# Kernel optimization log

Measured on AMD Instinct MI355X. Metric: run time of the kernel, lower is better.

## Reference

```python
import jax, jax.numpy as jnp
import numpy as np

N_LEVELS = 16
N_FEATS = 2
LOG2_T = 19
TABLE_SIZE = 2 ** LOG2_T
BASE_RES = 16
PER_LEVEL_SCALE = 1.3819
N_PTS = 524288
# per-level grid resolutions (static)
RESOLUTIONS = np.floor(BASE_RES * PER_LEVEL_SCALE ** np.arange(N_LEVELS)).astype(np.float32)
# NGP spatial hash primes for 2D
PRIME0 = np.uint32(1)
PRIME1 = np.uint32(2654435761)
# corner offsets for bilinear interp: (0,0),(0,1),(1,0),(1,1)
CORNER_OFFS = np.array([[0, 0], [0, 1], [1, 0], [1, 1]], dtype=np.uint32)


def setup_inputs() -> dict:
    key = jax.random.key(0)
    k1, k2 = jax.random.split(key)
    pts = jax.random.uniform(k1, (N_PTS, 3), dtype=jnp.float32)  # coords in [0,1]
    # 3 planes x L levels x T entries x F features, small init like NGP (1e-4)
    tables = jax.random.normal(k2, (3, N_LEVELS, TABLE_SIZE, N_FEATS), dtype=jnp.float32) * 1e-4
    return {"pts": pts, "tables": tables}


def _encode_plane(coords, table):
    # coords: [N,2] in [0,1]; table: [L,T,F]
    L, T, F = table.shape
    res = jnp.asarray(RESOLUTIONS)  # [L]
    scaled = coords[None, :, :] * res[:, None, None]  # [L,N,2]
    x0 = jnp.floor(scaled)
    frac = scaled - x0  # [L,N,2]
    x0u = x0.astype(jnp.uint32)
    offs = jnp.asarray(CORNER_OFFS)  # [4,2]
    corners = x0u[:, :, None, :] + offs[None, None, :, :]  # [L,N,4,2]
    # NGP spatial hash with uint32 wraparound, then mod table size
    h = (corners[..., 0] * PRIME0) ^ (corners[..., 1] * PRIME1)  # [L,N,4] uint32
    idx = (h % jnp.uint32(T)).astype(jnp.int32)  # [L,N,4]
    feats = table[jnp.arange(L)[:, None, None], idx]  # [L,N,4,F]
    # bilinear weights: product over dims of frac (offset=1) or 1-frac (offset=0)
    fo = offs.astype(coords.dtype)  # [4,2]
    w = jnp.prod(jnp.where(fo[None, None] > 0, frac[:, :, None, :], 1.0 - frac[:, :, None, :]), axis=-1)  # [L,N,4]
    out = jnp.einsum('lnc,lncf->lnf', w, feats)  # [L,N,F]
    return out.transpose(1, 0, 2).reshape(coords.shape[0], L * F)  # [N, L*F]


def reference(pts, tables):
    # coordinate-pair planes: combinations of (0,1,2) taken 2 at a time
    coo_combs = [(0, 1), (0, 2), (1, 2)]
    interp_space = 1.0
    for ci, comb in enumerate(coo_combs):
        interp_space = interp_space * _encode_plane(pts[:, list(comb)], tables[ci])
    return interp_space  # [N, 32]
```

## Files before the change

### kernel.cpp

```cpp
#include <hip/hip_runtime.h>
#include <stdint.h>


#define NPTS   524288u
#define TSIZE  524288u
#define TMASK  0x7FFFFu
#define PRIME1 2654435761u

__constant__ float c_res[16] = {
    16.f, 22.f, 30.f, 42.f, 58.f, 80.f, 111.f, 153.f,
    212.f, 294.f, 406.f, 561.f, 775.f, 1072.f, 1481.f, 2047.f
};
__constant__ int c_resiLow[12] = {16, 22, 30, 42, 58, 80, 111, 153, 212, 294, 406, 561};

__global__ __launch_bounds__(256) void k_pack(
    const float* __restrict__ pts, float2* __restrict__ pts2,
    uint32_t* __restrict__ hist)
{
    const uint32_t b = blockIdx.x, t = threadIdx.x;
    if (b == 2048u) {
        if (t < 256u) { hist[t] = 0u; hist[256u + t] = 0u; hist[512u + t] = 0u; }
        return;
    }
    const uint32_t pt = b * 256u + t;
    const float x = pts[pt * 3u + 0u];
    const float y = pts[pt * 3u + 1u];
    const float z = pts[pt * 3u + 2u];
    pts2[            pt] = make_float2(x, y);
    pts2[NPTS      + pt] = make_float2(x, z);
    pts2[2u * NPTS + pt] = make_float2(y, z);
}

__global__ __launch_bounds__(256) void k_hist(
    const float2* __restrict__ pts2, uint32_t* __restrict__ hist)
{
    __shared__ uint32_t lh[256];
    const uint32_t b = blockIdx.x, t = threadIdx.x;
    const uint32_t plane = b >> 6, chunk = b & 63u;
    lh[t] = 0u;
    __syncthreads();
    const float2* __restrict__ pp = pts2 + (size_t)plane * NPTS;
    const uint32_t pt0 = chunk * 8192u + t;
    for (uint32_t k = 0; k < 32u; ++k) {
        const float2 c = pp[pt0 + k * 256u];
        const uint32_t bx = min(15u, (uint32_t)(c.x * 16.f));
        const uint32_t by = min(15u, (uint32_t)(c.y * 16.f));
        atomicAdd(&lh[bx * 16u + by], 1u);
    }
    __syncthreads();
    atomicAdd(&hist[plane * 256u + t], lh[t]);
}

__global__ __launch_bounds__(256) void k_scan(
    const uint32_t* __restrict__ hist,
    uint32_t* __restrict__ base, uint32_t* __restrict__ cursor)
{
    __shared__ uint32_t su[256];
    const uint32_t t = threadIdx.x;
    for (uint32_t p = 0; p < 3u; ++p) {
        const uint32_t h = hist[p * 256u + t];
        su[t] = h;
        __syncthreads();
        for (uint32_t off = 1u; off < 256u; off <<= 1) {
            uint32_t v = 0u;
            if (t >= off) v = su[t - off];
            __syncthreads();
            su[t] += v;
            __syncthreads();
        }
        const uint32_t ex = su[t] - h;
        base[p * 256u + t] = ex;
        cursor[p * 256u + t] = ex;
        __syncthreads();
    }
}

__global__ __launch_bounds__(256) void k_scatter(
    const float2* __restrict__ pts2, uint32_t* __restrict__ cursor,
    float4* __restrict__ sort16)
{
    __shared__ uint32_t lcnt[256], gb[256], lc2[256];
    const uint32_t b = blockIdx.x, t = threadIdx.x;
    const uint32_t plane = b >> 6, chunk = b & 63u;
    lcnt[t] = 0u; lc2[t] = 0u;
    __syncthreads();
    const float2* __restrict__ pp = pts2 + (size_t)plane * NPTS;
    const uint32_t pt0 = chunk * 8192u + t;
    for (uint32_t k = 0; k < 32u; ++k) {
        const float2 c = pp[pt0 + k * 256u];
        const uint32_t bb = min(15u, (uint32_t)(c.x * 16.f)) * 16u
                          + min(15u, (uint32_t)(c.y * 16.f));
        atomicAdd(&lcnt[bb], 1u);
    }
    __syncthreads();
    gb[t] = atomicAdd(&cursor[plane * 256u + t], lcnt[t]);
    __syncthreads();
    float4* __restrict__ sp = sort16 + (size_t)plane * NPTS;
    for (uint32_t k = 0; k < 32u; ++k) {
        const uint32_t pt = pt0 + k * 256u;
        const float2 c = pp[pt];
        const uint32_t bb = min(15u, (uint32_t)(c.x * 16.f)) * 16u
                          + min(15u, (uint32_t)(c.y * 16.f));
        const uint32_t r = atomicAdd(&lc2[bb], 1u);
        sp[gb[bb] + r] = make_float4(c.x, c.y, __uint_as_float(pt), 0.f);
    }
}

__global__ __launch_bounds__(256) void k_low(
    const float2* __restrict__ tab, const float4* __restrict__ sort16,
    const uint32_t* __restrict__ hist, const uint32_t* __restrict__ base,
    float2* __restrict__ ws2)
{
    __shared__ float2 sm[4000];
    __shared__ uint32_t Poff[12], Pu0[12], Pu1[12], Pcols[12], Prows[12];
    const uint32_t b = blockIdx.x, t = threadIdx.x;
    const uint32_t plane = b >> 8, bucket = b & 255u;
    const uint32_t bx = bucket >> 4, by = bucket & 15u;

    if (t == 0u) {
        uint32_t off = 0u;
        for (uint32_t l = 0; l < 12u; ++l) {
            const int R = c_resiLow[l];
            const int u0s = max(0, (int)(((int)bx * R) >> 4) - 1);
            const int u0e = min(R, (int)((((int)bx + 1) * R) >> 4) + 2);
            const int u1s = max(0, (int)(((int)by * R) >> 4) - 1);
            const int u1e = min(R, (int)((((int)by + 1) * R) >> 4) + 2);
            const uint32_t rows = (uint32_t)(u0e - u0s + 1);
            const uint32_t cols = (uint32_t)(u1e - u1s + 1);
            Poff[l] = off; Pu0[l] = (uint32_t)u0s; Pu1[l] = (uint32_t)u1s;
            Pcols[l] = cols; Prows[l] = rows;
            off += rows * cols;
        }
    }
    __syncthreads();

    for (uint32_t l = 0; l < 12u; ++l) {
        const uint32_t E = Prows[l] * Pcols[l];
        const uint32_t cols = Pcols[l], u0s = Pu0[l], u1s = Pu1[l];
        const uint32_t tb = (plane * 16u + l) * TSIZE;
        for (uint32_t i = t; i < E; i += 256u) {
            const uint32_t cx = u0s + i / cols;
            const uint32_t cy = u1s + i - (i / cols) * cols;
            sm[Poff[l] + i] = tab[tb + ((cx ^ (cy * PRIME1)) & TMASK)];
        }
    }
    __syncthreads();

    const uint32_t count = hist[plane * 256u + bucket];
    const uint32_t start = base[plane * 256u + bucket];
    const float4* __restrict__ sp = sort16 + (size_t)plane * NPTS;
    float4* __restrict__ w4 = (float4*)ws2;

    for (uint32_t i = t; i < count; i += 256u) {
        const float4 f = sp[start + i];
        const float c0 = f.x, c1 = f.y;
        const uint32_t orig = __float_as_uint(f.z);
        float2 acc[12];
#pragma unroll
        for (int l = 0; l < 12; ++l) {
            const float res = c_res[l];
            const float s0 = c0 * res;
            const float s1 = c1 * res;
            const float f0 = floorf(s0);
            const float f1 = floorf(s1);
            const float r0 = s0 - f0;
            const float r1 = s1 - f1;
            const uint32_t u0 = (uint32_t)f0, u1 = (uint32_t)f1;
            const uint32_t ci = Poff[l] + (u0 - Pu0[l]) * Pcols[l] + (u1 - Pu1[l]);
            const float2 q00 = sm[ci];
            const float2 q01 = sm[ci + 1u];
            const float2 q10 = sm[ci + Pcols[l]];
            const float2 q11 = sm[ci + Pcols[l] + 1u];
            const float w00 = (1.f - r0) * (1.f - r1);
            const float w01 = (1.f - r0) * r1;
            const float w10 = r0 * (1.f - r1);
            const float w11 = r0 * r1;
            acc[l] = make_float2(
                w00 * q00.x + w01 * q01.x + w10 * q10.x + w11 * q11.x,
                w00 * q00.y + w01 * q01.y + w10 * q10.y + w11 * q11.y);
        }
        const size_t d = (size_t)orig * 18u + (size_t)plane * 6u;
        w4[d + 0] = make_float4(acc[0].x, acc[0].y, acc[1].x, acc[1].y);
        w4[d + 1] = make_float4(acc[2].x, acc[2].y, acc[3].x, acc[3].y);
        w4[d + 2] = make_float4(acc[4].x, acc[4].y, acc[5].x, acc[5].y);
        w4[d + 3] = make_float4(acc[6].x, acc[6].y, acc[7].x, acc[7].y);
        w4[d + 4] = make_float4(acc[8].x, acc[8].y, acc[9].x, acc[9].y);
        w4[d + 5] = make_float4(acc[10].x, acc[10].y, acc[11].x, acc[11].y);
    }
}

__global__ __launch_bounds__(256) void k_hi(
    const float2* __restrict__ pts2, const float2* __restrict__ tab,
    float2* __restrict__ wsH)
{
    const uint32_t b = blockIdx.x, t = threadIdx.x;
    const uint32_t xcd = b & 7u;
    const uint32_t s   = b >> 3;
    uint32_t g, chunk;
    if (s < 512u) { g = xcd; chunk = s; }
    else { g = 8u + (xcd >> 1); chunk = ((xcd & 1u) << 8) + (s - 512u); }
    const uint32_t plane = g % 3u;
    const uint32_t lvl   = 12u + g / 3u;
    const uint32_t gabs  = plane * 16u + lvl;
    const float    res   = c_res[lvl];
    const uint32_t tb    = gabs * TSIZE;
    const float4* __restrict__ tab4 = (const float4*)tab;
    const uint32_t b4    = gabs * (TSIZE / 2u);
    const float2* __restrict__ pp = pts2 + (size_t)plane * NPTS;
    const uint32_t pt0   = chunk * 1024u + t;

    float4 P0[4], P1[4];
    float2 Q0[4], Q1[4];
    float  r0[4], r1[4];
    uint32_t sel0[4], sel1[4], oddm[4];

#pragma unroll
    for (int k = 0; k < 4; ++k) {
        const uint32_t pt = pt0 + (uint32_t)k * 256u;
        const float2 c2 = pp[pt];
        const float s0 = c2.x * res;
        const float s1 = c2.y * res;
        const float f0 = floorf(s0);
        const float f1 = floorf(s1);
        r0[k] = s0 - f0;
        r1[k] = s1 - f1;
        const uint32_t u0  = (uint32_t)f0;
        const uint32_t hy0 = (uint32_t)f1 * PRIME1;
        const uint32_t hy1 = hy0 + PRIME1;
        const uint32_t i00 = ( u0        ^ hy0) & TMASK;
        const uint32_t i01 = ( u0        ^ hy1) & TMASK;
        const uint32_t i10 = ((u0 + 1u)  ^ hy0) & TMASK;
        const uint32_t i11 = ((u0 + 1u)  ^ hy1) & TMASK;
        sel0[k] = i00 & 1u;
        sel1[k] = i01 & 1u;
        oddm[k] = u0 & 1u;
        P0[k] = tab4[b4 + (i00 >> 1)];
        P1[k] = tab4[b4 + (i01 >> 1)];
        Q0[k] = make_float2(0.f, 0.f);
        Q1[k] = make_float2(0.f, 0.f);
        if (oddm[k]) {
            Q0[k] = tab[tb + i10];
            Q1[k] = tab[tb + i11];
        }
    }
#pragma unroll
    for (int k = 0; k < 4; ++k) {
        const uint32_t pt = pt0 + (uint32_t)k * 256u;
        const float2 lo0 = make_float2(P0[k].x, P0[k].y);
        const float2 hi0 = make_float2(P0[k].z, P0[k].w);
        const float2 lo1 = make_float2(P1[k].x, P1[k].y);
        const float2 hi1 = make_float2(P1[k].z, P1[k].w);
        const float2 t00 = sel0[k] ? hi0 : lo0;
        const float2 t01 = sel1[k] ? hi1 : lo1;
        const float2 t10 = oddm[k] ? Q0[k] : (sel0[k] ? lo0 : hi0);
        const float2 t11 = oddm[k] ? Q1[k] : (sel1[k] ? lo1 : hi1);
        const float w00 = (1.f - r0[k]) * (1.f - r1[k]);
        const float w01 = (1.f - r0[k]) * r1[k];
        const float w10 = r0[k] * (1.f - r1[k]);
        const float w11 = r0[k] * r1[k];
        wsH[(size_t)g * NPTS + pt] = make_float2(
            w00 * t00.x + w01 * t01.x + w10 * t10.x + w11 * t11.x,
            w00 * t00.y + w01 * t01.y + w10 * t10.y + w11 * t11.y);
    }
}

__global__ __launch_bounds__(256) void k_comb(
    const float2* __restrict__ ws2, const float2* __restrict__ wsH,
    float2* __restrict__ out)
{
    __shared__ float2 s2[2304];
    __shared__ float2 sh[768];
    const uint32_t b = blockIdx.x, t = threadIdx.x;
    const uint32_t pt0 = b * 64u;
    const float2* __restrict__ src = ws2 + (size_t)pt0 * 36u;
    for (uint32_t i = t; i < 2304u; i += 256u) s2[i] = src[i];
    for (uint32_t i = t; i < 768u; i += 256u) {
        const uint32_t j = i >> 6, p = i & 63u;
        sh[i] = wsH[(size_t)j * NPTS + pt0 + p];
    }
    __syncthreads();
#pragma unroll
    for (uint32_t k = 0; k < 4u; ++k) {
        const uint32_t e = t + k * 256u;
        const uint32_t pt = e >> 4, l = e & 15u;
        float2 v;
        if (l < 12u) {
            const float2 a = s2[pt * 36u + l];
            const float2 bb = s2[pt * 36u + 12u + l];
            const float2 c = s2[pt * 36u + 24u + l];
            v = make_float2(a.x * bb.x * c.x, a.y * bb.y * c.y);
        } else {
            const uint32_t j0 = (l - 12u) * 3u;
            const float2 a = sh[j0 * 64u + pt];
            const float2 bb = sh[(j0 + 1u) * 64u + pt];
            const float2 c = sh[(j0 + 2u) * 64u + pt];
            v = make_float2(a.x * bb.x * c.x, a.y * bb.y * c.y);
        }
        out[(size_t)(pt0 + pt) * 16u + l] = v;
    }
}

template <int P, bool FIRST>
__global__ __launch_bounds__(256) void kplane_pass(
    const float* __restrict__ pts, const float2* __restrict__ tab,
    float2* __restrict__ ws)
{
    const uint32_t b     = blockIdx.x;
    const uint32_t xcd   = b & 7u;
    const uint32_t s     = b >> 3;
    const uint32_t gi    = s >> 11;
    const uint32_t chunk = s & 2047u;
    const uint32_t lvl   = gi * 8u + xcd;
    const uint32_t pt    = chunk * 256u + threadIdx.x;
    constexpr int c0 = (P == 2) ? 1 : 0;
    constexpr int c1 = (P == 0) ? 1 : 2;
    const float a0  = pts[pt * 3u + c0];
    const float a1  = pts[pt * 3u + c1];
    const float res = c_res[lvl];
    const float s0 = a0 * res;
    const float s1 = a1 * res;
    const float f0 = floorf(s0);
    const float f1 = floorf(s1);
    const float r0 = s0 - f0;
    const float r1 = s1 - f1;
    const uint32_t u0 = (uint32_t)f0;
    const uint32_t hy0  = (uint32_t)f1 * PRIME1;
    const uint32_t hy1  = hy0 + PRIME1;
    const uint32_t base = ((uint32_t)P * 16u + lvl) * TSIZE;
    const float2 t00 = tab[base + (( u0       ^ hy0) & TMASK)];
    const float2 t01 = tab[base + (( u0       ^ hy1) & TMASK)];
    const float2 t10 = tab[base + (((u0 + 1u) ^ hy0) & TMASK)];
    const float2 t11 = tab[base + (((u0 + 1u) ^ hy1) & TMASK)];
    const float w00 = (1.f - r0) * (1.f - r1);
    const float w01 = (1.f - r0) * r1;
    const float w10 = r0 * (1.f - r1);
    const float w11 = r0 * r1;
    const float e0 = w00 * t00.x + w01 * t01.x + w10 * t10.x + w11 * t11.x;
    const float e1 = w00 * t00.y + w01 * t01.y + w10 * t10.y + w11 * t11.y;
    const uint32_t widx = lvl * NPTS + pt;
    if (FIRST) {
        ws[widx] = make_float2(e0, e1);
    } else {
        const float2 prev = ws[widx];
        ws[widx] = make_float2(prev.x * e0, prev.y * e1);
    }
}

__global__ __launch_bounds__(256) void kplane_transpose(
    const float2* __restrict__ ws, float2* __restrict__ out)
{
    const uint32_t tid = blockIdx.x * 256u + threadIdx.x;
    const uint32_t lvl = tid & 15u;
    const uint32_t pt  = tid >> 4;
    out[tid] = ws[lvl * NPTS + pt];
}

__global__ __launch_bounds__(256) void kplane_mono(
    const float* __restrict__ pts, const float2* __restrict__ tab,
    float2* __restrict__ out)
{
    const uint32_t tid = blockIdx.x * 256u + threadIdx.x;
    const uint32_t pt  = tid >> 4;
    const uint32_t lvl = tid & 15u;
    const float x = pts[pt * 3u + 0u];
    const float y = pts[pt * 3u + 1u];
    const float z = pts[pt * 3u + 2u];
    const float res = c_res[lvl];
    const float a0[3] = {x, x, y};
    const float a1[3] = {y, z, z};
    float p0 = 1.f, p1 = 1.f;
#pragma unroll
    for (int pl = 0; pl < 3; ++pl) {
        const float s0 = a0[pl] * res;
        const float s1 = a1[pl] * res;
        const float f0 = floorf(s0);
        const float f1 = floorf(s1);
        const float r0 = s0 - f0;
        const float r1 = s1 - f1;
        const uint32_t u0 = (uint32_t)f0;
        const uint32_t hy0 = (uint32_t)f1 * PRIME1;
        const uint32_t hy1 = hy0 + PRIME1;
        const uint32_t base = ((uint32_t)pl * 16u + lvl) * TSIZE;
        const float2 t00 = tab[base + (( u0       ^ hy0) & TMASK)];
        const float2 t01 = tab[base + (( u0       ^ hy1) & TMASK)];
        const float2 t10 = tab[base + (((u0 + 1u) ^ hy0) & TMASK)];
        const float2 t11 = tab[base + (((u0 + 1u) ^ hy1) & TMASK)];
        const float w00 = (1.f - r0) * (1.f - r1);
        const float w01 = (1.f - r0) * r1;
        const float w10 = r0 * (1.f - r1);
        const float w11 = r0 * r1;
        p0 *= w00 * t00.x + w01 * t01.x + w10 * t10.x + w11 * t11.x;
        p1 *= w00 * t00.y + w01 * t01.y + w10 * t10.y + w11 * t11.y;
    }
    out[pt * 16u + lvl] = make_float2(p0, p1);
}

extern "C" void kernel_launch(void* const* d_in, const int* in_sizes, int n_in,
                              void* d_out, int out_size, void* d_ws, size_t ws_size,
                              hipStream_t stream) {
    const float*  pts = (const float*)d_in[0];
    const float2* tab = (const float2*)d_in[1];
    float2*       out = (float2*)d_out;

    const size_t wsA = (size_t)48 * NPTS * sizeof(float2);
    const size_t wsB = (size_t)16 * NPTS * sizeof(float2);
    dim3 block256(256u);

    if (ws_size >= wsA) {
        float2*   pts2   = (float2*)d_out;
        float4*   sort16 = (float4*)((char*)d_out + (size_t)3 * NPTS * 8u);
        uint32_t* hist   = (uint32_t*)((char*)d_out + (size_t)3 * NPTS * 24u);
        uint32_t* bse    = hist + 768;
        uint32_t* cursor = hist + 1536;
        float2* ws2 = (float2*)d_ws;
        float2* wsH = ws2 + (size_t)36 * NPTS;

        hipLaunchKernelGGL(k_pack,    dim3(2049u), block256, 0, stream, pts, pts2, hist);
        hipLaunchKernelGGL(k_hist,    dim3(192u),  block256, 0, stream, pts2, hist);
        hipLaunchKernelGGL(k_scan,    dim3(1u),    block256, 0, stream, hist, bse, cursor);
        hipLaunchKernelGGL(k_scatter, dim3(192u),  block256, 0, stream, pts2, cursor, sort16);
        hipLaunchKernelGGL(k_low,     dim3(768u),  block256, 0, stream, tab, sort16, hist, bse, ws2);
        hipLaunchKernelGGL(k_hi,      dim3(6144u), block256, 0, stream, pts2, tab, wsH);
        hipLaunchKernelGGL(k_comb,    dim3(NPTS / 64u), block256, 0, stream, ws2, wsH, out);
    } else if (ws_size >= wsB) {
        float2* ws = (float2*)d_ws;
        dim3 grid(16u * (NPTS / 256u));
        hipLaunchKernelGGL((kplane_pass<0, true >), grid, block256, 0, stream, pts, tab, ws);
        hipLaunchKernelGGL((kplane_pass<1, false>), grid, block256, 0, stream, pts, tab, ws);
        hipLaunchKernelGGL((kplane_pass<2, false>), grid, block256, 0, stream, pts, tab, ws);
        dim3 tgrid((NPTS * 16u) / 256u);
        hipLaunchKernelGGL(kplane_transpose, tgrid, block256, 0, stream, ws, out);
    } else {
        dim3 grid((NPTS * 16u) / 256u);
        hipLaunchKernelGGL(kplane_mono, grid, block256, 0, stream, pts, tab, out);
    }
}
```

Baseline: 252.4 us.

## Fuse histogram into pack, scan into scatter, and low/high level passes

```diff
diff --git a/kernel.cpp b/kernel.cpp
--- a/kernel.cpp
+++ b/kernel.cpp
@@ -13,15 +13,14 @@
 };
 __constant__ int c_resiLow[12] = {16, 22, 30, 42, 58, 80, 111, 153, 212, 294, 406, 561};
 
-__global__ __launch_bounds__(256) void k_pack(
+__global__ __launch_bounds__(256) void k_packhist(
     const float* __restrict__ pts, float2* __restrict__ pts2,
     uint32_t* __restrict__ hist)
 {
+    __shared__ uint32_t lh[768];
     const uint32_t b = blockIdx.x, t = threadIdx.x;
-    if (b == 2048u) {
-        if (t < 256u) { hist[t] = 0u; hist[256u + t] = 0u; hist[512u + t] = 0u; }
-        return;
-    }
+    lh[t] = 0u; lh[t + 256u] = 0u; lh[t + 512u] = 0u;
+    __syncthreads();
     const uint32_t pt = b * 256u + t;
     const float x = pts[pt * 3u + 0u];
     const float y = pts[pt * 3u + 1u];
@@ -29,61 +28,36 @@
     pts2[            pt] = make_float2(x, y);
     pts2[NPTS      + pt] = make_float2(x, z);
     pts2[2u * NPTS + pt] = make_float2(y, z);
-}
-
-__global__ __launch_bounds__(256) void k_hist(
-    const float2* __restrict__ pts2, uint32_t* __restrict__ hist)
-{
-    __shared__ uint32_t lh[256];
+    const uint32_t bx = min(15u, (uint32_t)(x * 16.f));
+    const uint32_t by = min(15u, (uint32_t)(y * 16.f));
+    const uint32_t bz = min(15u, (uint32_t)(z * 16.f));
+    atomicAdd(&lh[         bx * 16u + by], 1u);
+    atomicAdd(&lh[256u +   bx * 16u + bz], 1u);
+    atomicAdd(&lh[512u +   by * 16u + bz], 1u);
+    __syncthreads();
+    if (lh[t])        atomicAdd(&hist[t],        lh[t]);
+    if (lh[t + 256u]) atomicAdd(&hist[t + 256u], lh[t + 256u]);
+    if (lh[t + 512u]) atomicAdd(&hist[t + 512u], lh[t + 512u]);
+}
+
+__global__ __launch_bounds__(256) void k_scatter(
+    const float2* __restrict__ pts2, const uint32_t* __restrict__ hist,
+    uint32_t* __restrict__ cursor, float4* __restrict__ sort16)
+{
+    __shared__ uint32_t su[256], lcnt[256], gb[256], lc2[256];
     const uint32_t b = blockIdx.x, t = threadIdx.x;
     const uint32_t plane = b >> 6, chunk = b & 63u;
-    lh[t] = 0u;
-    __syncthreads();
-    const float2* __restrict__ pp = pts2 + (size_t)plane * NPTS;
-    const uint32_t pt0 = chunk * 8192u + t;
-    for (uint32_t k = 0; k < 32u; ++k) {
-        const float2 c = pp[pt0 + k * 256u];
-        const uint32_t bx = min(15u, (uint32_t)(c.x * 16.f));
-        const uint32_t by = min(15u, (uint32_t)(c.y * 16.f));
-        atomicAdd(&lh[bx * 16u + by], 1u);
-    }
-    __syncthreads();
-    atomicAdd(&hist[plane * 256u + t], lh[t]);
-}
-
-__global__ __launch_bounds__(256) void k_scan(
-    const uint32_t* __restrict__ hist,
-    uint32_t* __restrict__ base, uint32_t* __restrict__ cursor)
-{
-    __shared__ uint32_t su[256];
-    const uint32_t t = threadIdx.x;
-    for (uint32_t p = 0; p < 3u; ++p) {
-        const uint32_t h = hist[p * 256u + t];
-        su[t] = h;
-        __syncthreads();
-        for (uint32_t off = 1u; off < 256u; off <<= 1) {
-            uint32_t v = 0u;
-            if (t >= off) v = su[t - off];
-            __syncthreads();
-            su[t] += v;
-            __syncthreads();
-        }
-        const uint32_t ex = su[t] - h;
-        base[p * 256u + t] = ex;
-        cursor[p * 256u + t] = ex;
-        __syncthreads();
-    }
-}
-
-__global__ __launch_bounds__(256) void k_scatter(
-    const float2* __restrict__ pts2, uint32_t* __restrict__ cursor,
-    float4* __restrict__ sort16)
-{
-    __shared__ uint32_t lcnt[256], gb[256], lc2[256];
-    const uint32_t b = blockIdx.x, t = threadIdx.x;
-    const uint32_t plane = b >> 6, chunk = b & 63u;
-    lcnt[t] = 0u; lc2[t] = 0u;
-    __syncthreads();
+    const uint32_t h = hist[plane * 256u + t];
+    su[t] = h; lcnt[t] = 0u; lc2[t] = 0u;
+    __syncthreads();
+    for (uint32_t off = 1u; off < 256u; off <<= 1) {
+        uint32_t v = 0u;
+        if (t >= off) v = su[t - off];
+        __syncthreads();
+        su[t] += v;
+        __syncthreads();
+    }
+    const uint32_t mybase = su[t] - h;
     const float2* __restrict__ pp = pts2 + (size_t)plane * NPTS;
     const uint32_t pt0 = chunk * 8192u + t;
     for (uint32_t k = 0; k < 32u; ++k) {
@@ -93,7 +67,7 @@
         atomicAdd(&lcnt[bb], 1u);
     }
     __syncthreads();
-    gb[t] = atomicAdd(&cursor[plane * 256u + t], lcnt[t]);
+    gb[t] = mybase + atomicAdd(&cursor[plane * 256u + t], lcnt[t]);
     __syncthreads();
     float4* __restrict__ sp = sort16 + (size_t)plane * NPTS;
     for (uint32_t k = 0; k < 32u; ++k) {
@@ -106,96 +80,114 @@
     }
 }
 
-__global__ __launch_bounds__(256) void k_low(
-    const float2* __restrict__ tab, const float4* __restrict__ sort16,
-    const uint32_t* __restrict__ hist, const uint32_t* __restrict__ base,
-    float2* __restrict__ ws2)
+__global__ __launch_bounds__(256) void k_lowhi(
+    const float2* __restrict__ pts2, const float4* __restrict__ sort16,
+    const uint32_t* __restrict__ hist, const float2* __restrict__ tab,
+    float2* __restrict__ ws2, float2* __restrict__ wsH)
 {
     __shared__ float2 sm[4000];
-    __shared__ uint32_t Poff[12], Pu0[12], Pu1[12], Pcols[12], Prows[12];
     const uint32_t b = blockIdx.x, t = threadIdx.x;
-    const uint32_t plane = b >> 8, bucket = b & 255u;
-    const uint32_t bx = bucket >> 4, by = bucket & 15u;
-
-    if (t == 0u) {
-        uint32_t off = 0u;
+
+    if (b < 768u) {
+        const uint32_t plane  = b >> 8;
+        const uint32_t bucket = b & 255u;
+        const uint32_t bx = bucket >> 4, by = bucket & 15u;
+
+        uint32_t* su = (uint32_t*)sm;
+        const uint32_t h = hist[plane * 256u + t];
+        su[t] = h;
+        __syncthreads();
+        for (uint32_t off = 1u; off < 256u; off <<= 1) {
+            uint32_t v = 0u;
+            if (t >= off) v = su[t - off];
+            __syncthreads();
+            su[t] += v;
+            __syncthreads();
+        }
+        const uint32_t cntB  = hist[plane * 256u + bucket];
+        const uint32_t start = su[bucket] - cntB;
+        __syncthreads();
+
+        uint32_t* Pm = (uint32_t*)(sm + 3968);
+        if (t == 0u) {
+            uint32_t off = 0u;
+            for (uint32_t l = 0; l < 12u; ++l) {
+                const int R = c_resiLow[l];
+                const int u0s = max(0, (int)((bx * (uint32_t)R) >> 4) - 1);
+                const int u0e = min(R, (int)(((bx + 1u) * (uint32_t)R) >> 4) + 2);
+                const int u1s = max(0, (int)((by * (uint32_t)R) >> 4) - 1);
+                const int u1e = min(R, (int)(((by + 1u) * (uint32_t)R) >> 4) + 2);
+                const uint32_t rows = (uint32_t)(u0e - u0s + 1);
+                const uint32_t cols = (uint32_t)(u1e - u1s + 1);
+                Pm[l] = off; Pm[12u + l] = (uint32_t)u0s;
+                Pm[24u + l] = (uint32_t)u1s; Pm[36u + l] = cols;
+                Pm[48u + l] = rows;
+                off += rows * cols;
+            }
+        }
+        __syncthreads();
+
         for (uint32_t l = 0; l < 12u; ++l) {
-            const int R = c_resiLow[l];
-            const int u0s = max(0, (int)(((int)bx * R) >> 4) - 1);
-            const int u0e = min(R, (int)((((int)bx + 1) * R) >> 4) + 2);
-            const int u1s = max(0, (int)(((int)by * R) >> 4) - 1);
-            const int u1e = min(R, (int)((((int)by + 1) * R) >> 4) + 2);
-            const uint32_t rows = (uint32_t)(u0e - u0s + 1);
-            const uint32_t cols = (uint32_t)(u1e - u1s + 1);
-            Poff[l] = off; Pu0[l] = (uint32_t)u0s; Pu1[l] = (uint32_t)u1s;
-            Pcols[l] = cols; Prows[l] = rows;
-            off += rows * cols;
-        }
-    }
-    __syncthreads();
-
-    for (uint32_t l = 0; l < 12u; ++l) {
-        const uint32_t E = Prows[l] * Pcols[l];
-        const uint32_t cols = Pcols[l], u0s = Pu0[l], u1s = Pu1[l];
-        const uint32_t tb = (plane * 16u + l) * TSIZE;
-        for (uint32_t i = t; i < E; i += 256u) {
-            const uint32_t cx = u0s + i / cols;
-            const uint32_t cy = u1s + i - (i / cols) * cols;
-            sm[Poff[l] + i] = tab[tb + ((cx ^ (cy * PRIME1)) & TMASK)];
-        }
-    }
-    __syncthreads();
-
-    const uint32_t count = hist[plane * 256u + bucket];
-    const uint32_t start = base[plane * 256u + bucket];
-    const float4* __restrict__ sp = sort16 + (size_t)plane * NPTS;
-    float4* __restrict__ w4 = (float4*)ws2;
-
-    for (uint32_t i = t; i < count; i += 256u) {
-        const float4 f = sp[start + i];
-        const float c0 = f.x, c1 = f.y;
-        const uint32_t orig = __float_as_uint(f.z);
-        float2 acc[12];
+            const uint32_t off  = Pm[l];
+            const uint32_t u0s  = Pm[12u + l], u1s = Pm[24u + l];
+            const uint32_t cols = Pm[36u + l], rows = Pm[48u + l];
+            const uint32_t E    = rows * cols;
+            const uint32_t tb   = (plane * 16u + l) * TSIZE;
+            for (uint32_t i = t; i < E; i += 256u) {
+                const uint32_t r  = i / cols;
+                const uint32_t cx = u0s + r;
+                const uint32_t cy = u1s + (i - r * cols);
+                sm[off + i] = tab[tb + ((cx ^ (cy * PRIME1)) & TMASK)];
+            }
+        }
+        __syncthreads();
+
+        const float4* __restrict__ sp = sort16 + (size_t)plane * NPTS;
+        float4* __restrict__ w4 = (float4*)ws2;
+        for (uint32_t i = t; i < cntB; i += 256u) {
+            const float4 f = sp[start + i];
+            const float c0 = f.x, c1 = f.y;
+            const uint32_t orig = __float_as_uint(f.z);
+            float2 acc[12];
 #pragma unroll
-        for (int l = 0; l < 12; ++l) {
-            const float res = c_res[l];
-            const float s0 = c0 * res;
-            const float s1 = c1 * res;
-            const float f0 = floorf(s0);
-            const float f1 = floorf(s1);
-            const float r0 = s0 - f0;
-            const float r1 = s1 - f1;
-            const uint32_t u0 = (uint32_t)f0, u1 = (uint32_t)f1;
-            const uint32_t ci = Poff[l] + (u0 - Pu0[l]) * Pcols[l] + (u1 - Pu1[l]);
-            const float2 q00 = sm[ci];
-            const float2 q01 = sm[ci + 1u];
-            const float2 q10 = sm[ci + Pcols[l]];
-            const float2 q11 = sm[ci + Pcols[l] + 1u];
-            const float w00 = (1.f - r0) * (1.f - r1);
-            const float w01 = (1.f - r0) * r1;
-            const float w10 = r0 * (1.f - r1);
-            const float w11 = r0 * r1;
-            acc[l] = make_float2(
-                w00 * q00.x + w01 * q01.x + w10 * q10.x + w11 * q11.x,
-                w00 * q00.y + w01 * q01.y + w10 * q10.y + w11 * q11.y);
-        }
-        const size_t d = (size_t)orig * 18u + (size_t)plane * 6u;
-        w4[d + 0] = make_float4(acc[0].x, acc[0].y, acc[1].x, acc[1].y);
-        w4[d + 1] = make_float4(acc[2].x, acc[2].y, acc[3].x, acc[3].y);
-        w4[d + 2] = make_float4(acc[4].x, acc[4].y, acc[5].x, acc[5].y);
-        w4[d + 3] = make_float4(acc[6].x, acc[6].y, acc[7].x, acc[7].y);
-        w4[d + 4] = make_float4(acc[8].x, acc[8].y, acc[9].x, acc[9].y);
-        w4[d + 5] = make_float4(acc[10].x, acc[10].y, acc[11].x, acc[11].y);
-    }
-}
-
-__global__ __launch_bounds__(256) void k_hi(
-    const float2* __restrict__ pts2, const float2* __restrict__ tab,
-    float2* __restrict__ wsH)
-{
-    const uint32_t b = blockIdx.x, t = threadIdx.x;
-    const uint32_t xcd = b & 7u;
-    const uint32_t s   = b >> 3;
+            for (int l = 0; l < 12; ++l) {
+                const float res = c_res[l];
+                const float s0 = c0 * res;
+                const float s1 = c1 * res;
+                const float f0 = floorf(s0);
+                const float f1 = floorf(s1);
+                const float r0 = s0 - f0;
+                const float r1 = s1 - f1;
+                const uint32_t u0 = (uint32_t)f0, u1 = (uint32_t)f1;
+                const uint32_t cols = Pm[36u + l];
+                const uint32_t ci = Pm[l] + (u0 - Pm[12u + l]) * cols
+                                  + (u1 - Pm[24u + l]);
+                const float2 q00 = sm[ci];
+                const float2 q01 = sm[ci + 1u];
+                const float2 q10 = sm[ci + cols];
+                const float2 q11 = sm[ci + cols + 1u];
+                const float w00 = (1.f - r0) * (1.f - r1);
+                const float w01 = (1.f - r0) * r1;
+                const float w10 = r0 * (1.f - r1);
+                const float w11 = r0 * r1;
+                acc[l] = make_float2(
+                    w00 * q00.x + w01 * q01.x + w10 * q10.x + w11 * q11.x,
+                    w00 * q00.y + w01 * q01.y + w10 * q10.y + w11 * q11.y);
+            }
+            const size_t d = (size_t)orig * 18u + (size_t)plane * 6u;
+            w4[d + 0] = make_float4(acc[0].x, acc[0].y, acc[1].x, acc[1].y);
+            w4[d + 1] = make_float4(acc[2].x, acc[2].y, acc[3].x, acc[3].y);
+            w4[d + 2] = make_float4(acc[4].x, acc[4].y, acc[5].x, acc[5].y);
+            w4[d + 3] = make_float4(acc[6].x, acc[6].y, acc[7].x, acc[7].y);
+            w4[d + 4] = make_float4(acc[8].x, acc[8].y, acc[9].x, acc[9].y);
+            w4[d + 5] = make_float4(acc[10].x, acc[10].y, acc[11].x, acc[11].y);
+        }
+        return;
+    }
+
+    const uint32_t hb  = b - 768u;
+    const uint32_t xcd = hb & 7u;
+    const uint32_t s   = hb >> 3;
     uint32_t g, chunk;
     if (s < 512u) { g = xcd; chunk = s; }
     else { g = 8u + (xcd >> 1); chunk = ((xcd & 1u) << 8) + (s - 512u); }
@@ -285,15 +277,15 @@
         const uint32_t pt = e >> 4, l = e & 15u;
         float2 v;
         if (l < 12u) {
-            const float2 a = s2[pt * 36u + l];
+            const float2 a  = s2[pt * 36u + l];
             const float2 bb = s2[pt * 36u + 12u + l];
-            const float2 c = s2[pt * 36u + 24u + l];
+            const float2 c  = s2[pt * 36u + 24u + l];
             v = make_float2(a.x * bb.x * c.x, a.y * bb.y * c.y);
         } else {
             const uint32_t j0 = (l - 12u) * 3u;
-            const float2 a = sh[j0 * 64u + pt];
+            const float2 a  = sh[j0 * 64u + pt];
             const float2 bb = sh[(j0 + 1u) * 64u + pt];
-            const float2 c = sh[(j0 + 2u) * 64u + pt];
+            const float2 c  = sh[(j0 + 2u) * 64u + pt];
             v = make_float2(a.x * bb.x * c.x, a.y * bb.y * c.y);
         }
         out[(size_t)(pt0 + pt) * 16u + l] = v;
@@ -408,20 +400,21 @@
 
     if (ws_size >= wsA) {
         float2*   pts2   = (float2*)d_out;
-        float4*   sort16 = (float4*)((char*)d_out + (size_t)3 * NPTS * 8u);
-        uint32_t* hist   = (uint32_t*)((char*)d_out + (size_t)3 * NPTS * 24u);
-        uint32_t* bse    = hist + 768;
-        uint32_t* cursor = hist + 1536;
+        float4*   sort16 = (float4*)(pts2 + (size_t)3 * NPTS);
+        uint32_t* hist   = (uint32_t*)(sort16 + (size_t)3 * NPTS);
+        uint32_t* cursor = hist + 768;
         float2* ws2 = (float2*)d_ws;
         float2* wsH = ws2 + (size_t)36 * NPTS;
 
-        hipLaunchKernelGGL(k_pack,    dim3(2049u), block256, 0, stream, pts, pts2, hist);
-        hipLaunchKernelGGL(k_hist,    dim3(192u),  block256, 0, stream, pts2, hist);
-        hipLaunchKernelGGL(k_scan,    dim3(1u),    block256, 0, stream, hist, bse, cursor);
-        hipLaunchKernelGGL(k_scatter, dim3(192u),  block256, 0, stream, pts2, cursor, sort16);
-        hipLaunchKernelGGL(k_low,     dim3(768u),  block256, 0, stream, tab, sort16, hist, bse, ws2);
-        hipLaunchKernelGGL(k_hi,      dim3(6144u), block256, 0, stream, pts2, tab, wsH);
-        hipLaunchKernelGGL(k_comb,    dim3(NPTS / 64u), block256, 0, stream, ws2, wsH, out);
+        hipMemsetAsync(hist, 0, 1536u * sizeof(uint32_t), stream);
+        hipLaunchKernelGGL(k_packhist, dim3(2048u), block256, 0, stream,
+                           pts, pts2, hist);
+        hipLaunchKernelGGL(k_scatter,  dim3(192u),  block256, 0, stream,
+                           pts2, hist, cursor, sort16);
+        hipLaunchKernelGGL(k_lowhi,    dim3(6912u), block256, 0, stream,
+                           pts2, sort16, hist, tab, ws2, wsH);
+        hipLaunchKernelGGL(k_comb,     dim3(NPTS / 64u), block256, 0, stream,
+                           ws2, wsH, out);
     } else if (ws_size >= wsB) {
         float2* ws = (float2*)d_ws;
         dim3 grid(16u * (NPTS / 256u));
```

Result: slower. 282.1 us (+11.8%).
